# Kernel optimization log

Hardware: AMD Instinct MI355X
Metric: run time of the kernel (lower is better)

The kernel has to match this reference:

```python
import jax, jax.numpy as jnp
import numpy as np


def _conv2d(x, w, b):
    # 3x3 conv, stride 1, pad 1, NCHW
    y = jax.lax.conv_general_dilated(x, w, (1, 1), ((1, 1), (1, 1)),
                                     dimension_numbers=('NCHW', 'OIHW', 'NCHW'))
    return y + b[None, :, None, None]


def _up2(x):
    return jnp.repeat(jnp.repeat(x, 2, axis=2), 2, axis=3)


def _mdconv(x, w, b, ow, ob):
    # Modulated deformable conv v2 (mmcv semantics): 3x3, stride 1, pad 1,
    # dilation 1, deformable_groups=1. Offsets/mask predicted by conv_offset,
    # out = chunk3 -> (o1, o2, mask); offset = cat(o1, o2); mask = sigmoid(mask).
    B, Cin, H, W = x.shape
    off = _conv2d(x, ow, ob)                        # [B,27,H,W]
    o1, o2, m = jnp.split(off, 3, axis=1)
    offs = jnp.concatenate([o1, o2], axis=1)        # [B,18,H,W]
    dy, dx = offs[:, 0::2], offs[:, 1::2]           # [B,9,H,W] (dy,dx interleaved per kernel pt)
    mask = jax.nn.sigmoid(m)                        # [B,9,H,W]
    ky, kx = jnp.meshgrid(jnp.arange(3), jnp.arange(3), indexing='ij')
    # sampling positions: p0 + pn + offset (pad=1)
    py = jnp.arange(H, dtype=x.dtype)[None, None, :, None] - 1.0 + ky.reshape(1, 9, 1, 1) + dy
    px = jnp.arange(W, dtype=x.dtype)[None, None, None, :] - 1.0 + kx.reshape(1, 9, 1, 1) + dx
    y0 = jnp.floor(py); x0 = jnp.floor(px)
    wy1 = py - y0; wx1 = px - x0
    y0i = y0.astype(jnp.int32); x0i = x0.astype(jnp.int32)
    flat = x.reshape(B, Cin, H * W)

    def gather(yi, xi):
        valid = ((yi >= 0) & (yi < H) & (xi >= 0) & (xi < W)).astype(x.dtype)  # zero padding
        idx = jnp.clip(yi, 0, H - 1) * W + jnp.clip(xi, 0, W - 1)             # [B,9,H,W]
        g = jax.vmap(lambda f, i: f[:, i])(flat, idx)                          # [B,Cin,9,H,W]
        return g * valid[:, None]

    val = (gather(y0i, x0i) * ((1 - wy1) * (1 - wx1))[:, None]
           + gather(y0i, x0i + 1) * ((1 - wy1) * wx1)[:, None]
           + gather(y0i + 1, x0i) * (wy1 * (1 - wx1))[:, None]
           + gather(y0i + 1, x0i + 1) * (wy1 * wx1)[:, None])
    cols = val * mask[:, None]                      # [B,Cin,9,H,W]
    out = jnp.einsum('ock,bckhw->bohw', w.reshape(w.shape[0], Cin, 9), cols)
    return out + b[None, :, None, None]


def setup_inputs() -> dict:
    key = jax.random.key(0)
    ks = jax.random.split(key, 24)
    C = 256
    sizes = [(96, 96), (48, 48), (24, 24), (12, 12)]
    d = {}
    for i, (h, w) in enumerate(sizes):
        d[f'x{i}'] = jax.random.normal(ks[i], (2, C, h, w), dtype=jnp.float32)
    for i in range(4):
        d[f'w{i}'] = jax.random.normal(ks[4 + i], (C, C, 3, 3), dtype=jnp.float32) * 0.02
        d[f'b{i}'] = jax.random.normal(ks[8 + i], (C,), dtype=jnp.float32) * 0.02
    for i in range(1, 4):
        d[f'ow{i}'] = jax.random.normal(ks[12 + i], (27, C, 3, 3), dtype=jnp.float32) * 0.01
        d[f'ob{i}'] = jax.random.normal(ks[16 + i], (27,), dtype=jnp.float32) * 0.01
    return d


def reference(x0, x1, x2, x3, w0, w1, w2, w3, b0, b1, b2, b3,
              ow1, ow2, ow3, ob1, ob2, ob3):
    # tdm_convs[3] called with level=1 -> deform; the same-size nearest interpolate is identity
    t3 = _mdconv(x3, w3, b3, ow3, ob3)
    # i=3: tdm_convs[2](2, x2 + up(t3)) -> deform
    t2 = _mdconv(x2 + _up2(t3), w2, b2, ow2, ob2)
    # i=2: tdm_convs[1](1, x1 + up(t2)) -> deform
    t1 = _mdconv(x1 + _up2(t2), w1, b1, ow1, ob1)
    # i=1: tdm_convs[0](0, x0 + up(t1)) -> level 0 < start_level -> plain conv
    t0 = _conv2d(x0 + _up2(t1), w0, b0)
    return (t0, t1, t2, t3)
```

## Files before the change

kernel.cpp:

```cpp
#include <hip/hip_runtime.h>
#include <math.h>

__device__ __forceinline__ ushort f2bf(float f) {
    unsigned int u = __float_as_uint(f);
    u += 0x7FFFu + ((u >> 16) & 1u);
    return (ushort)(u >> 16);
}

typedef __attribute__((address_space(1))) const unsigned int guint;
typedef __attribute__((address_space(3))) unsigned int luint;
__device__ __forceinline__ void gload_lds16(const void* g, void* l) {
    __builtin_amdgcn_global_load_lds((guint*)g, (luint*)l, 16, 0, 0);
}

template<int N>
__device__ __forceinline__ void waitvm() {
    if constexpr (N == 0)      asm volatile("s_waitcnt vmcnt(0)" ::: "memory");
    else if constexpr (N == 3) asm volatile("s_waitcnt vmcnt(3)" ::: "memory");
    else if constexpr (N == 4) asm volatile("s_waitcnt vmcnt(4)" ::: "memory");
    else                       asm volatile("s_waitcnt vmcnt(6)" ::: "memory");
}

using bfrag = __attribute__((ext_vector_type(8))) short;
using f4    = __attribute__((ext_vector_type(4))) float;

__device__ __forceinline__ void bf8_to_f(uint4 v, float* o) {
    unsigned int u[4] = {v.x, v.y, v.z, v.w};
    #pragma unroll
    for (int i = 0; i < 4; ++i) {
        o[2 * i]     = __uint_as_float(u[i] << 16);
        o[2 * i + 1] = __uint_as_float(u[i] & 0xFFFF0000u);
    }
}

__device__ __forceinline__ void xs_body(void* smem,
    const float* __restrict__ x, const float* __restrict__ prev,
    ushort* __restrict__ xs, int H, int W, int bx, int by, int bz)
{
    ushort (*tile)[72] = (ushort(*)[72])smem;
    const int HW = H * W, W2 = W >> 1;
    int b = bz, c0 = by * 32, hw0 = bx * 64;
    const float* xb = x + ((size_t)b * 256 + c0) * HW;
    const float* pb = prev ? prev + ((size_t)b * 256 + c0) * (HW >> 2) : nullptr;

    int hwl = threadIdx.x & 63, cl0 = threadIdx.x >> 6;
    int hw = hw0 + hwl;
    bool ok = hw < HW;
    int hwc = ok ? hw : HW - 1;
    int h = hwc / W, w = hwc - h * W;
    int pidx = (h >> 1) * W2 + (w >> 1);
    #pragma unroll
    for (int p = 0; p < 8; ++p) {
        int cl = p * 4 + cl0;
        float v = 0.f;
        if (ok) {
            v = xb[(size_t)cl * HW + hw];
            if (pb) v += pb[(size_t)cl * (HW >> 2) + pidx];
        }
        tile[cl][hwl] = f2bf(v);
    }
    __syncthreads();
    int hwl2 = threadIdx.x >> 2, cc = (threadIdx.x & 3) * 8;
    int hw2 = hw0 + hwl2;
    if (hw2 < HW) {
        ushort vals[8];
        #pragma unroll
        for (int j = 0; j < 8; ++j) vals[j] = tile[cc + j][hwl2];
        *(uint4*)&xs[((size_t)b * HW + hw2) * 256 + c0 + cc] = *(uint4*)vals;
    }
}

struct ProArgs {
    const float* wsrc[7];
    ushort*      wdst[7];
    float*       outp[3];
    const float* bias[3];
    float*       zbase;
    int          z4;
    const float* x3;
    ushort*      xs3;
};
__global__ __launch_bounds__(256) void prolog_kernel(ProArgs a) {
    __shared__ __align__(16) char smem[18432];
    const int tid = threadIdx.x;
    int vb = blockIdx.x;
    if (vb < 277) {
        const float* src; ushort* dst; int M, m0;
        if (vb < 256) { src = a.wsrc[vb >> 6]; dst = a.wdst[vb >> 6]; M = 256; m0 = (vb & 63) * 4; }
        else { int u = vb - 256; src = a.wsrc[4 + u / 7]; dst = a.wdst[4 + u / 7]; M = 27; m0 = (u % 7) * 4; }
        ushort* lt = (ushort*)smem;
        #pragma unroll
        for (int i = 0; i < 9; ++i) {
            int fi = i * 256 + tid;
            if (m0 + fi / 576 < M) {
                float4 v = *(const float4*)(src + ((size_t)m0 * 2304 + (size_t)fi * 4));
                lt[fi * 4 + 0] = f2bf(v.x); lt[fi * 4 + 1] = f2bf(v.y);
                lt[fi * 4 + 2] = f2bf(v.z); lt[fi * 4 + 3] = f2bf(v.w);
            }
        }
        __syncthreads();
        for (int ch = tid; ch < 1152; ch += 256) {
            int m4 = ch / 288, rem = ch - m4 * 288;
            int r = rem >> 5, c8 = rem & 31;
            int m = m0 + m4;
            if (m < M) {
                ushort vals[8];
                #pragma unroll
                for (int j = 0; j < 8; ++j) vals[j] = lt[m4 * 2304 + (c8 * 8 + j) * 9 + r];
                *(uint4*)&dst[(size_t)m * 2304 + r * 256 + c8 * 8] = *(uint4*)vals;
            }
        }
    } else if (vb < 1789) {
        float* op; const float* bp; int HW, base;
        if (vb < 1429)      { op = a.outp[0]; bp = a.bias[0]; HW = 2304; base = vb - 277; }
        else if (vb < 1717) { op = a.outp[1]; bp = a.bias[1]; HW = 576;  base = vb - 1429; }
        else                { op = a.outp[2]; bp = a.bias[2]; HW = 144;  base = vb - 1717; }
        int i = base * 256 + tid;
        if (i < 128 * HW) {
            int e = i << 2;
            int m = (e / HW) & 255;
            float v = bp[m];
            *(float4*)&op[e] = float4{v, v, v, v};
        }
    } else if (vb < 1949) {
        int i = (vb - 1789) * 256 + tid;
        if (i < a.z4) ((float4*)a.zbase)[i] = float4{0.f, 0.f, 0.f, 0.f};
    } else {
        int v = vb - 1949;
        xs_body(smem, a.x3, nullptr, a.xs3, 12, 12, v % 3, (v / 3) & 7, v / 24);
    }
}

__global__ __launch_bounds__(256) void xs_nhwc(
    const float* __restrict__ x, const float* __restrict__ prev,
    ushort* __restrict__ xs, int H, int W)
{
    __shared__ __align__(16) char smem[32 * 72 * 2];
    xs_body(smem, x, prev, xs, H, W, blockIdx.x, blockIdx.y, blockIdx.z);
}

__global__ __launch_bounds__(256) void sampling_kernel(
    const ushort* __restrict__ xs, const float* __restrict__ off,
    const float* __restrict__ ob, ushort* __restrict__ cols,
    int H, int W)
{
    __shared__ float4 gw[8][9];
    __shared__ int4   go[8][9];
    const int HW = H * W;
    const int b = blockIdx.z;
    const int hw0 = blockIdx.x * 8;
    const int tid = threadIdx.x;
    const float* offb = off + (size_t)b * 27 * HW;
    const ushort* xb = xs + (size_t)b * HW * 256;

    if (tid < 72) {
        int hwl = tid / 9, k = tid - hwl * 9;
        int hw = hw0 + hwl; if (hw >= HW) hw = HW - 1;
        int h = hw / W, w = hw - h * W;
        float dy = offb[(size_t)(2 * k) * HW + hw] + ob[2 * k];
        float dx = offb[(size_t)(2 * k + 1) * HW + hw] + ob[2 * k + 1];
        float mv = offb[(size_t)(18 + k) * HW + hw] + ob[18 + k];
        float mk = 1.0f / (1.0f + __expf(-mv));
        float py = (float)h - 1.0f + (float)(k / 3) + dy;
        float px = (float)w - 1.0f + (float)(k % 3) + dx;
        float y0f = floorf(py), x0f = floorf(px);
        float wy = py - y0f, wx = px - x0f;
        int y0 = (int)y0f, x0i = (int)x0f;
        int y1 = y0 + 1, x1 = x0i + 1;
        bool vy0 = (y0 >= 0) & (y0 < H), vy1 = (y1 >= 0) & (y1 < H);
        bool vx0 = (x0i >= 0) & (x0i < W), vx1 = (x1 >= 0) & (x1 < W);
        float w00 = (1.f - wy) * (1.f - wx) * ((vy0 & vx0) ? mk : 0.f);
        float w01 = (1.f - wy) * wx        * ((vy0 & vx1) ? mk : 0.f);
        float w10 = wy * (1.f - wx)        * ((vy1 & vx0) ? mk : 0.f);
        float w11 = wy * wx                * ((vy1 & vx1) ? mk : 0.f);
        int cy0 = min(max(y0, 0), H - 1), cy1 = min(max(y1, 0), H - 1);
        int cx0 = min(max(x0i, 0), W - 1), cx1 = min(max(x1, 0), W - 1);
        gw[hwl][k] = float4{w00, w01, w10, w11};
        go[hwl][k] = int4{(cy0 * W + cx0) << 8, (cy0 * W + cx1) << 8,
                          (cy1 * W + cx0) << 8, (cy1 * W + cx1) << 8};
    }
    __syncthreads();

    int hwl = tid >> 5, cb = (tid & 31) * 8;
    int hw = hw0 + hwl;
    if (hw >= HW) return;
    ushort* colp = cols + ((size_t)b * HW + hw) * 2304 + cb;

    #pragma unroll
    for (int k = 0; k < 9; ++k) {
        float4 wv = gw[hwl][k];
        int4   ov = go[hwl][k];
        float f00[8], f01[8], f10[8], f11[8];
        bf8_to_f(*(const uint4*)(xb + ov.x + cb), f00);
        bf8_to_f(*(const uint4*)(xb + ov.y + cb), f01);
        bf8_to_f(*(const uint4*)(xb + ov.z + cb), f10);
        bf8_to_f(*(const uint4*)(xb + ov.w + cb), f11);
        unsigned int pk[4];
        #pragma unroll
        for (int t = 0; t < 4; ++t) {
            float lo = f00[2 * t] * wv.x + f01[2 * t] * wv.y +
                       f10[2 * t] * wv.z + f11[2 * t] * wv.w;
            float hi = f00[2 * t + 1] * wv.x + f01[2 * t + 1] * wv.y +
                       f10[2 * t + 1] * wv.z + f11[2 * t + 1] * wv.w;
            pk[t] = (unsigned int)f2bf(lo) | ((unsigned int)f2bf(hi) << 16);
        }
        *(uint4*)(colp + k * 256) = make_uint4(pk[0], pk[1], pk[2], pk[3]);
    }
}

template<bool IMPLICIT, bool SPLITK, int BM, int MT, int MO>
__global__ __launch_bounds__(256) void mfma_gemm(
    const ushort* __restrict__ A, const float* __restrict__ bias,
    const ushort* __restrict__ Bt, const ushort* __restrict__ zeros,
    float* __restrict__ outp, int N, int H, int W, int kchunk)
{
    constexpr int AL = BM / 32;
    constexpr int AI = BM / 32;
    constexpr int S  = AL + 2;
    __shared__ __align__(16) ushort As[2][BM * 64];
    __shared__ __align__(16) ushort Bs[2][64 * 64];
    const int b  = blockIdx.z;
    const int m0 = (blockIdx.y % MT) * BM;
    const int kt0 = (blockIdx.y / MT) * kchunk;
    const int n0 = blockIdx.x * 64;
    const int tid  = threadIdx.x;
    const int lane = tid & 63;
    const int wv   = tid >> 6;
    const int wm = wv & 1, wn = wv >> 1;

    const ushort* Bb = IMPLICIT ? Bt + (size_t)b * N * 256
                                : Bt + (size_t)b * (size_t)N * 2304;

    const int sc8 = ((tid & 7) ^ ((tid >> 3) & 7)) * 8;
    const int srow = tid >> 3;
    int bn[2], bh[2], bw[2];
    #pragma unroll
    for (int j = 0; j < 2; ++j) {
        int n = n0 + j * 32 + srow; if (n >= N) n = N - 1;
        bn[j] = n; bh[j] = n / W; bw[j] = n - bh[j] * W;
    }

    auto stage = [&](int kt, int bi) {
        #pragma unroll
        for (int i = 0; i < AL; ++i) {
            gload_lds16(A + (size_t)(m0 + i * 32 + srow) * 2304 + kt + sc8,
                        (char*)As[bi] + (size_t)(i * 256 + (tid & ~63)) * 16);
        }
        if (!IMPLICIT) {
            #pragma unroll
            for (int j = 0; j < 2; ++j)
                gload_lds16(Bb + (size_t)bn[j] * 2304 + kt + sc8,
                            (char*)Bs[bi] + (size_t)(j * 256 + (tid & ~63)) * 16);
        } else {
            int r = kt >> 8, c0k = kt & 255;
            int ry = r / 3 - 1, rx = r - (r / 3) * 3 - 1;
            #pragma unroll
            for (int j = 0; j < 2; ++j) {
                int ih = bh[j] + ry, iw = bw[j] + rx;
                const ushort* src = (ih >= 0 && ih < H && iw >= 0 && iw < W)
                    ? Bb + (((size_t)(ih * W + iw)) << 8) + c0k + sc8
                    : zeros;
                gload_lds16(src, (char*)Bs[bi] + (size_t)(j * 256 + (tid & ~63)) * 16);
            }
        }
    };

    const int fq = (lane >> 4);
    const int fv = (lane & 7);
    f4 acc[AI][2] = {};

    const int nit = kchunk >> 6;
    stage(kt0, 0);
    if (nit > 1) stage(kt0 + 64, 1);
    for (int it = 0; it < nit; ++it) {
        if (it + 1 < nit) waitvm<S>(); else waitvm<0>();
        __builtin_amdgcn_s_barrier();
        __builtin_amdgcn_sched_barrier(0);
        const ushort* as = As[it & 1];
        const ushort* bs = Bs[it & 1];
        bfrag af[2][AI], bf[2][2];
        #pragma unroll
        for (int kh = 0; kh < 2; ++kh) {
            int ch = ((kh * 4 + fq) ^ fv) * 8;
            #pragma unroll
            for (int i = 0; i < AI; ++i)
                af[kh][i] = *(const bfrag*)&as[(wm * (BM / 2) + i * 16 + (lane & 15)) * 64 + ch];
            #pragma unroll
            for (int j = 0; j < 2; ++j)
                bf[kh][j] = *(const bfrag*)&bs[(wn * 32 + j * 16 + (lane & 15)) * 64 + ch];
        }
        asm volatile("s_waitcnt lgkmcnt(0)" ::: "memory");
        __builtin_amdgcn_s_barrier();
        __builtin_amdgcn_sched_barrier(0);
        if (it + 2 < nit) stage(kt0 + (it + 2) * 64, it & 1);
        #pragma unroll
        for (int kh = 0; kh < 2; ++kh)
            #pragma unroll
            for (int i = 0; i < AI; ++i)
                #pragma unroll
                for (int j = 0; j < 2; ++j)
                    acc[i][j] = __builtin_amdgcn_mfma_f32_16x16x32_bf16(
                        af[kh][i], bf[kh][j], acc[i][j], 0, 0, 0);
    }

    const int mb = m0 + wm * (BM / 2), nb = n0 + wn * 32;
    #pragma unroll
    for (int i = 0; i < AI; ++i) {
        int mrow = mb + i * 16 + (lane >> 4) * 4;
        #pragma unroll
        for (int j = 0; j < 2; ++j) {
            int n = nb + j * 16 + (lane & 15);
            if (n < N) {
                #pragma unroll
                for (int t = 0; t < 4; ++t) {
                    int m = mrow + t;
                    if (MO == 256 || m < MO) {
                        if (SPLITK)
                            atomicAdd(&outp[((size_t)b * MO + m) * N + n], acc[i][j][t]);
                        else
                            outp[((size_t)b * MO + m) * N + n] = acc[i][j][t] + bias[m];
                    }
                }
            }
        }
    }
}

extern "C" void kernel_launch(void* const* d_in, const int* in_sizes, int n_in,
                              void* d_out, int out_size, void* d_ws, size_t ws_size,
                              hipStream_t stream)
{
    const float* x[4]   = {(const float*)d_in[0], (const float*)d_in[1],
                           (const float*)d_in[2], (const float*)d_in[3]};
    const float* wgt[4] = {(const float*)d_in[4], (const float*)d_in[6],
                           (const float*)d_in[8], (const float*)d_in[10]};
    const float* bia[4] = {(const float*)d_in[5], (const float*)d_in[7],
                           (const float*)d_in[9], (const float*)d_in[11]};
    const float* owt[4] = {nullptr, (const float*)d_in[12],
                           (const float*)d_in[14], (const float*)d_in[16]};
    const float* obv[4] = {nullptr, (const float*)d_in[13],
                           (const float*)d_in[15], (const float*)d_in[17]};

    const int B = 2;
    const int Hs[4] = {96, 48, 24, 12};
    const int HWs[4] = {96 * 96, 48 * 48, 24 * 24, 12 * 12};

    float* out = (float*)d_out;
    size_t outOff[4];
    outOff[0] = 0;
    outOff[1] = outOff[0] + (size_t)B * 256 * HWs[0];
    outOff[2] = outOff[1] + (size_t)B * 256 * HWs[1];
    outOff[3] = outOff[2] + (size_t)B * 256 * HWs[2];

    char* ws = (char*)d_ws;
    size_t off = 0;
    auto carve = [&](size_t bytes) { void* p = ws + off; off = (off + bytes + 255) & ~(size_t)255; return p; };
    ushort* wbf[4];
    ushort* owbf[4] = {nullptr, nullptr, nullptr, nullptr};
    for (int i = 0; i < 4; ++i) wbf[i] = (ushort*)carve((size_t)256 * 2304 * 2);
    for (int i = 1; i < 4; ++i) owbf[i] = (ushort*)carve((size_t)32 * 2304 * 2);
    ushort* cols = (ushort*)carve((size_t)B * HWs[1] * 2304 * 2);
    ushort* xsb[4];
    for (int i = 0; i < 4; ++i) xsb[i] = (ushort*)carve((size_t)B * 256 * HWs[i] * 2);
    int offElems = B * 27 * (HWs[1] + HWs[2] + HWs[3]);
    float* offbase = (float*)carve((size_t)offElems * 4 + 1024);
    ushort* zeros = (ushort*)(offbase + offElems);
    float* offbuf[4] = {nullptr,
                        offbase,
                        offbase + (size_t)B * 27 * HWs[1],
                        offbase + (size_t)B * 27 * (HWs[1] + HWs[2])};

    {
        ProArgs a;
        a.wsrc[0] = wgt[0]; a.wsrc[1] = wgt[1]; a.wsrc[2] = wgt[2]; a.wsrc[3] = wgt[3];
        a.wsrc[4] = owt[1]; a.wsrc[5] = owt[2]; a.wsrc[6] = owt[3];
        a.wdst[0] = wbf[0]; a.wdst[1] = wbf[1]; a.wdst[2] = wbf[2]; a.wdst[3] = wbf[3];
        a.wdst[4] = owbf[1]; a.wdst[5] = owbf[2]; a.wdst[6] = owbf[3];
        for (int i = 0; i < 3; ++i) {
            a.outp[i] = out + outOff[i + 1]; a.bias[i] = bia[i + 1];
        }
        a.zbase = offbase;
        a.z4 = (offElems * 4 + 1024) / 16;
        a.x3 = x[3];
        a.xs3 = xsb[3];
        prolog_kernel<<<dim3(1997), 256, 0, stream>>>(a);
    }

    const int oksplit[4] = {0, 6, 12, 18};
    const int ksplit[4]  = {1, 4, 6, 12};

    for (int lvl = 3; lvl >= 1; --lvl) {
        int H = Hs[lvl], W = H, HW = HWs[lvl];

        {
            dim3 grd((HW + 63) / 64, oksplit[lvl], B);
            mfma_gemm<true, true, 32, 1, 27><<<grd, 256, 0, stream>>>(
                owbf[lvl], nullptr, xsb[lvl], zeros, offbuf[lvl],
                HW, H, W, 2304 / oksplit[lvl]);
        }
        {
            dim3 grd((HW + 7) / 8, 1, B);
            sampling_kernel<<<grd, 256, 0, stream>>>(
                xsb[lvl], offbuf[lvl], obv[lvl], cols, H, W);
        }
        if (lvl == 1) {
            dim3 grd((HW + 63) / 64, 2 * 4, B);
            mfma_gemm<false, true, 128, 2, 256><<<grd, 256, 0, stream>>>(
                wbf[lvl], bia[lvl], cols, zeros, out + outOff[lvl],
                HW, H, W, 2304 / 4);
        } else {
            dim3 grd((HW + 63) / 64, 4 * ksplit[lvl], B);
            mfma_gemm<false, true, 64, 4, 256><<<grd, 256, 0, stream>>>(
                wbf[lvl], bia[lvl], cols, zeros, out + outOff[lvl],
                HW, H, W, 2304 / ksplit[lvl]);
        }
        {
            int Hn = Hs[lvl - 1];
            dim3 grd((HWs[lvl - 1] + 63) / 64, 8, B);
            xs_nhwc<<<grd, 256, 0, stream>>>(
                x[lvl - 1], out + outOff[lvl], xsb[lvl - 1], Hn, Hn);
        }
    }

    {
        dim3 grd((HWs[0] + 63) / 64, 2, 2);
        mfma_gemm<true, false, 128, 2, 256><<<grd, 256, 0, stream>>>(
            wbf[0], bia[0], xsb[0], zeros, out + outOff[0],
            HWs[0], Hs[0], Hs[0], 2304);
    }
}
```

Baseline: 243.3 us.

## Add 2-wave 128x64 MFMA GEMM with 64-wide K tiles and double buffering

Adds a new GEMM kernel that runs 128 threads (2 waves), each wave computing a 64x64 output tile. It uses 64-wide K steps with double-buffered LDS staging through global_load_lds and an XOR swizzle, and waits on vmcnt(12) so the next stage can stay in flight. The new kernel replaces the level-1 split-K GEMM and the final level-0 implicit conv. The aim is higher per-wave register reuse and fewer barriers per K unit, at the cost of fewer waves per block, more registers, and more LDS per block, which may lower occupancy.

```diff
diff --git a/kernel.cpp b/kernel.cpp
--- a/kernel.cpp
+++ b/kernel.cpp
@@ -15,10 +15,11 @@
 
 template<int N>
 __device__ __forceinline__ void waitvm() {
-    if constexpr (N == 0)      asm volatile("s_waitcnt vmcnt(0)" ::: "memory");
-    else if constexpr (N == 3) asm volatile("s_waitcnt vmcnt(3)" ::: "memory");
-    else if constexpr (N == 4) asm volatile("s_waitcnt vmcnt(4)" ::: "memory");
-    else                       asm volatile("s_waitcnt vmcnt(6)" ::: "memory");
+    if constexpr (N == 0)       asm volatile("s_waitcnt vmcnt(0)" ::: "memory");
+    else if constexpr (N == 3)  asm volatile("s_waitcnt vmcnt(3)" ::: "memory");
+    else if constexpr (N == 4)  asm volatile("s_waitcnt vmcnt(4)" ::: "memory");
+    else if constexpr (N == 6)  asm volatile("s_waitcnt vmcnt(6)" ::: "memory");
+    else                        asm volatile("s_waitcnt vmcnt(12)" ::: "memory");
 }
 
 using bfrag = __attribute__((ext_vector_type(8))) short;
@@ -326,6 +327,118 @@
     }
 }
 
+template<bool IMPLICIT, bool SPLITK>
+__global__ __launch_bounds__(128) void mfma_gemm2(
+    const ushort* __restrict__ A, const float* __restrict__ bias,
+    const ushort* __restrict__ Bt, const ushort* __restrict__ zeros,
+    float* __restrict__ outp, int N, int H, int W, int kchunk)
+{
+    __shared__ __align__(16) ushort As[2][128 * 64];
+    __shared__ __align__(16) ushort Bs[2][64 * 64];
+    const int b  = blockIdx.z;
+    const int m0 = (blockIdx.y & 1) * 128;
+    const int kt0 = (blockIdx.y >> 1) * kchunk;
+    const int n0 = blockIdx.x * 64;
+    const int tid  = threadIdx.x;
+    const int lane = tid & 63;
+    const int wv   = tid >> 6;
+
+    const ushort* Bb = IMPLICIT ? Bt + (size_t)b * N * 256
+                                : Bt + (size_t)b * (size_t)N * 2304;
+
+    const int sc8 = ((tid & 7) ^ ((tid >> 3) & 7)) * 8;
+    const int srow = tid >> 3;
+    int bn[4], bh[4], bw[4];
+    #pragma unroll
+    for (int j = 0; j < 4; ++j) {
+        int n = n0 + j * 16 + srow; if (n >= N) n = N - 1;
+        bn[j] = n; bh[j] = n / W; bw[j] = n - bh[j] * W;
+    }
+
+    auto stage = [&](int kt, int bi) {
+        #pragma unroll
+        for (int i = 0; i < 8; ++i) {
+            gload_lds16(A + (size_t)(m0 + i * 16 + srow) * 2304 + kt + sc8,
+                        (char*)As[bi] + (size_t)(i * 128 + (tid & ~63)) * 16);
+        }
+        if (!IMPLICIT) {
+            #pragma unroll
+            for (int j = 0; j < 4; ++j)
+                gload_lds16(Bb + (size_t)bn[j] * 2304 + kt + sc8,
+                            (char*)Bs[bi] + (size_t)(j * 128 + (tid & ~63)) * 16);
+        } else {
+            int r = kt >> 8, c0k = kt & 255;
+            int ry = r / 3 - 1, rx = r - (r / 3) * 3 - 1;
+            #pragma unroll
+            for (int j = 0; j < 4; ++j) {
+                int ih = bh[j] + ry, iw = bw[j] + rx;
+                const ushort* src = (ih >= 0 && ih < H && iw >= 0 && iw < W)
+                    ? Bb + (((size_t)(ih * W + iw)) << 8) + c0k + sc8
+                    : zeros;
+                gload_lds16(src, (char*)Bs[bi] + (size_t)(j * 128 + (tid & ~63)) * 16);
+            }
+        }
+    };
+
+    const int fq = (lane >> 4);
+    const int fv = (lane & 7);
+    f4 acc[4][4] = {};
+
+    const int nit = kchunk >> 6;
+    stage(kt0, 0);
+    if (nit > 1) stage(kt0 + 64, 1);
+    for (int it = 0; it < nit; ++it) {
+        if (it + 1 < nit) waitvm<12>(); else waitvm<0>();
+        __builtin_amdgcn_s_barrier();
+        __builtin_amdgcn_sched_barrier(0);
+        const ushort* as = As[it & 1];
+        const ushort* bs = Bs[it & 1];
+        bfrag af[2][4], bf[2][4];
+        #pragma unroll
+        for (int kh = 0; kh < 2; ++kh) {
+            int ch = ((kh * 4 + fq) ^ fv) * 8;
+            #pragma unroll
+            for (int i = 0; i < 4; ++i)
+                af[kh][i] = *(const bfrag*)&as[(wv * 64 + i * 16 + (lane & 15)) * 64 + ch];
+            #pragma unroll
+            for (int j = 0; j < 4; ++j)
+                bf[kh][j] = *(const bfrag*)&bs[(j * 16 + (lane & 15)) * 64 + ch];
+        }
+        asm volatile("s_waitcnt lgkmcnt(0)" ::: "memory");
+        __builtin_amdgcn_s_barrier();
+        __builtin_amdgcn_sched_barrier(0);
+        if (it + 2 < nit) stage(kt0 + (it + 2) * 64, it & 1);
+        #pragma unroll
+        for (int kh = 0; kh < 2; ++kh)
+            #pragma unroll
+            for (int i = 0; i < 4; ++i)
+                #pragma unroll
+                for (int j = 0; j < 4; ++j)
+                    acc[i][j] = __builtin_amdgcn_mfma_f32_16x16x32_bf16(
+                        af[kh][i], bf[kh][j], acc[i][j], 0, 0, 0);
+    }
+
+    const int mb = m0 + wv * 64;
+    #pragma unroll
+    for (int i = 0; i < 4; ++i) {
+        int mrow = mb + i * 16 + (lane >> 4) * 4;
+        #pragma unroll
+        for (int j = 0; j < 4; ++j) {
+            int n = n0 + j * 16 + (lane & 15);
+            if (n < N) {
+                #pragma unroll
+                for (int t = 0; t < 4; ++t) {
+                    int m = mrow + t;
+                    if (SPLITK)
+                        atomicAdd(&outp[((size_t)b * 256 + m) * N + n], acc[i][j][t]);
+                    else
+                        outp[((size_t)b * 256 + m) * N + n] = acc[i][j][t] + bias[m];
+                }
+            }
+        }
+    }
+}
+
 extern "C" void kernel_launch(void* const* d_in, const int* in_sizes, int n_in,
                               void* d_out, int out_size, void* d_ws, size_t ws_size,
                               hipStream_t stream)
@@ -405,7 +518,7 @@
         }
         if (lvl == 1) {
             dim3 grd((HW + 63) / 64, 2 * 4, B);
-            mfma_gemm<false, true, 128, 2, 256><<<grd, 256, 0, stream>>>(
+            mfma_gemm2<false, true><<<grd, 128, 0, stream>>>(
                 wbf[lvl], bia[lvl], cols, zeros, out + outOff[lvl],
                 HW, H, W, 2304 / 4);
         } else {
@@ -424,7 +537,7 @@
 
     {
         dim3 grd((HWs[0] + 63) / 64, 2, 2);
-        mfma_gemm<true, false, 128, 2, 256><<<grd, 256, 0, stream>>>(
+        mfma_gemm2<true, false><<<grd, 128, 0, stream>>>(
             wbf[0], bia[0], xsb[0], zeros, out + outOff[0],
             HWs[0], Hs[0], Hs[0], 2304);
     }
```

Result: slower. 250.5 us (+3.0%).

## Load GEMM operands directly from global into registers, bypassing LDS

Applied to the files above, without the earlier changes.

Replaces the LDS double-buffered staging (global_load_lds plus barriers) in the MFMA GEMM with direct per-lane global loads of the bf16 fragments into registers, double-buffered in registers (X/Y sets). This removes LDS traffic and the block-wide barriers. In exchange, warps no longer share operand tiles through LDS, so global and L2 traffic rise, with redundant loads across warps. Register pressure also goes up.

```diff
diff --git a/kernel.cpp b/kernel.cpp
--- a/kernel.cpp
+++ b/kernel.cpp
@@ -5,20 +5,6 @@
     unsigned int u = __float_as_uint(f);
     u += 0x7FFFu + ((u >> 16) & 1u);
     return (ushort)(u >> 16);
-}
-
-typedef __attribute__((address_space(1))) const unsigned int guint;
-typedef __attribute__((address_space(3))) unsigned int luint;
-__device__ __forceinline__ void gload_lds16(const void* g, void* l) {
-    __builtin_amdgcn_global_load_lds((guint*)g, (luint*)l, 16, 0, 0);
-}
-
-template<int N>
-__device__ __forceinline__ void waitvm() {
-    if constexpr (N == 0)      asm volatile("s_waitcnt vmcnt(0)" ::: "memory");
-    else if constexpr (N == 3) asm volatile("s_waitcnt vmcnt(3)" ::: "memory");
-    else if constexpr (N == 4) asm volatile("s_waitcnt vmcnt(4)" ::: "memory");
-    else                       asm volatile("s_waitcnt vmcnt(6)" ::: "memory");
 }
 
 using bfrag = __attribute__((ext_vector_type(8))) short;
@@ -214,11 +200,7 @@
     const ushort* __restrict__ Bt, const ushort* __restrict__ zeros,
     float* __restrict__ outp, int N, int H, int W, int kchunk)
 {
-    constexpr int AL = BM / 32;
     constexpr int AI = BM / 32;
-    constexpr int S  = AL + 2;
-    __shared__ __align__(16) ushort As[2][BM * 64];
-    __shared__ __align__(16) ushort Bs[2][64 * 64];
     const int b  = blockIdx.z;
     const int m0 = (blockIdx.y % MT) * BM;
     const int kt0 = (blockIdx.y / MT) * kchunk;
@@ -227,72 +209,60 @@
     const int lane = tid & 63;
     const int wv   = tid >> 6;
     const int wm = wv & 1, wn = wv >> 1;
+    const int fq = lane >> 4;
+    const int ln = lane & 15;
 
     const ushort* Bb = IMPLICIT ? Bt + (size_t)b * N * 256
                                 : Bt + (size_t)b * (size_t)N * 2304;
 
-    const int sc8 = ((tid & 7) ^ ((tid >> 3) & 7)) * 8;
-    const int srow = tid >> 3;
-    int bn[2], bh[2], bw[2];
+    const ushort* aptr[AI];
+    #pragma unroll
+    for (int i = 0; i < AI; ++i)
+        aptr[i] = A + (size_t)(m0 + wm * (BM / 2) + i * 16 + ln) * 2304 + kt0 + fq * 8;
+
+    int bh2[2], bw2[2];
+    const ushort* bptr[2];
     #pragma unroll
     for (int j = 0; j < 2; ++j) {
-        int n = n0 + j * 32 + srow; if (n >= N) n = N - 1;
-        bn[j] = n; bh[j] = n / W; bw[j] = n - bh[j] * W;
-    }
-
-    auto stage = [&](int kt, int bi) {
-        #pragma unroll
-        for (int i = 0; i < AL; ++i) {
-            gload_lds16(A + (size_t)(m0 + i * 32 + srow) * 2304 + kt + sc8,
-                        (char*)As[bi] + (size_t)(i * 256 + (tid & ~63)) * 16);
-        }
+        int n = n0 + wn * 32 + j * 16 + ln; if (n >= N) n = N - 1;
+        if (IMPLICIT) { int h = n / W; bh2[j] = h; bw2[j] = n - h * W; }
+        else          bptr[j] = Bb + (size_t)n * 2304 + kt0 + fq * 8;
+    }
+
+    auto loadA = [&](bfrag (&af)[2][AI], int it) {
+        #pragma unroll
+        for (int kh = 0; kh < 2; ++kh)
+            #pragma unroll
+            for (int i = 0; i < AI; ++i)
+                af[kh][i] = *(const bfrag*)(aptr[i] + it * 64 + kh * 32);
+    };
+    auto loadB = [&](bfrag (&bf)[2][2], int it) {
         if (!IMPLICIT) {
             #pragma unroll
-            for (int j = 0; j < 2; ++j)
-                gload_lds16(Bb + (size_t)bn[j] * 2304 + kt + sc8,
-                            (char*)Bs[bi] + (size_t)(j * 256 + (tid & ~63)) * 16);
+            for (int kh = 0; kh < 2; ++kh)
+                #pragma unroll
+                for (int j = 0; j < 2; ++j)
+                    bf[kh][j] = *(const bfrag*)(bptr[j] + it * 64 + kh * 32);
         } else {
-            int r = kt >> 8, c0k = kt & 255;
-            int ry = r / 3 - 1, rx = r - (r / 3) * 3 - 1;
+            int kg = kt0 + it * 64;
+            int r  = kg >> 8;
+            int c  = (kg & 255) + fq * 8;
+            int r3 = r / 3;
+            int ry = r3 - 1, rx = r - r3 * 3 - 1;
             #pragma unroll
             for (int j = 0; j < 2; ++j) {
-                int ih = bh[j] + ry, iw = bw[j] + rx;
-                const ushort* src = (ih >= 0 && ih < H && iw >= 0 && iw < W)
-                    ? Bb + (((size_t)(ih * W + iw)) << 8) + c0k + sc8
-                    : zeros;
-                gload_lds16(src, (char*)Bs[bi] + (size_t)(j * 256 + (tid & ~63)) * 16);
+                int ih = bh2[j] + ry, iw = bw2[j] + rx;
+                bool ok = (ih >= 0) && (ih < H) && (iw >= 0) && (iw < W);
+                const ushort* p = ok ? Bb + (((size_t)(ih * W + iw)) << 8) + c
+                                     : zeros + c;
+                bf[0][j] = *(const bfrag*)(p);
+                bf[1][j] = *(const bfrag*)(p + 32);
             }
         }
     };
 
-    const int fq = (lane >> 4);
-    const int fv = (lane & 7);
     f4 acc[AI][2] = {};
-
-    const int nit = kchunk >> 6;
-    stage(kt0, 0);
-    if (nit > 1) stage(kt0 + 64, 1);
-    for (int it = 0; it < nit; ++it) {
-        if (it + 1 < nit) waitvm<S>(); else waitvm<0>();
-        __builtin_amdgcn_s_barrier();
-        __builtin_amdgcn_sched_barrier(0);
-        const ushort* as = As[it & 1];
-        const ushort* bs = Bs[it & 1];
-        bfrag af[2][AI], bf[2][2];
-        #pragma unroll
-        for (int kh = 0; kh < 2; ++kh) {
-            int ch = ((kh * 4 + fq) ^ fv) * 8;
-            #pragma unroll
-            for (int i = 0; i < AI; ++i)
-                af[kh][i] = *(const bfrag*)&as[(wm * (BM / 2) + i * 16 + (lane & 15)) * 64 + ch];
-            #pragma unroll
-            for (int j = 0; j < 2; ++j)
-                bf[kh][j] = *(const bfrag*)&bs[(wn * 32 + j * 16 + (lane & 15)) * 64 + ch];
-        }
-        asm volatile("s_waitcnt lgkmcnt(0)" ::: "memory");
-        __builtin_amdgcn_s_barrier();
-        __builtin_amdgcn_sched_barrier(0);
-        if (it + 2 < nit) stage(kt0 + (it + 2) * 64, it & 1);
+    auto domfma = [&](bfrag (&af)[2][AI], bfrag (&bf)[2][2]) {
         #pragma unroll
         for (int kh = 0; kh < 2; ++kh)
             #pragma unroll
@@ -301,6 +271,19 @@
                 for (int j = 0; j < 2; ++j)
                     acc[i][j] = __builtin_amdgcn_mfma_f32_16x16x32_bf16(
                         af[kh][i], bf[kh][j], acc[i][j], 0, 0, 0);
+    };
+
+    bfrag afX[2][AI], bfX[2][2], afY[2][AI], bfY[2][2];
+    const int nit = kchunk >> 6;
+    loadA(afX, 0); loadB(bfX, 0);
+    int it = 0;
+    while (true) {
+        if (it + 1 < nit) { loadA(afY, it + 1); loadB(bfY, it + 1); }
+        domfma(afX, bfX);
+        if (++it == nit) break;
+        if (it + 1 < nit) { loadA(afX, it + 1); loadB(bfX, it + 1); }
+        domfma(afY, bfY);
+        if (++it == nit) break;
     }
 
     const int mb = m0 + wm * (BM / 2), nb = n0 + wn * 32;
```

Result: slower. 381.4 us (+56.8%).
